# Kernel tuning notes

Measured on AMD Instinct MI355X. Metric: run time of the kernel, lower is better.

## Reference

```python
import jax, jax.numpy as jnp
import numpy as np

D = 512      # d_model
H = 8        # num_heads
HD = D // H  # head_dim = 64
NI = 3       # num_inputs


def setup_inputs() -> dict:
    key = jax.random.key(0)
    ks = jax.random.split(key, 20)
    b, n, ni = 4, 8192, 4096
    s = 0.02
    inp = {
        "x": jax.random.normal(ks[0], (b, n, D), jnp.float32),
        "emb0": jax.random.normal(ks[1], (b, ni, D), jnp.float32),
        "emb1": jax.random.normal(ks[2], (b, ni, D), jnp.float32),
        "emb2": jax.random.normal(ks[3], (b, ni, D), jnp.float32),
        "Wq": jax.random.normal(ks[4], (D, D), jnp.float32) * s,
        "bq": jnp.zeros((D,), jnp.float32),
        "Wk": jax.random.normal(ks[5], (NI, D, D), jnp.float32) * s,
        "bk": jnp.zeros((NI, D), jnp.float32),
        "Wv": jax.random.normal(ks[6], (NI, D, D), jnp.float32) * s,
        "bv": jnp.zeros((NI, D), jnp.float32),
        "Wo": jax.random.normal(ks[7], (D, D), jnp.float32) * s,
        "bo": jnp.zeros((D,), jnp.float32),
        "mask0": jax.random.randint(ks[8], (b, ni), 0, 2).astype(bool),
        "mask1": jax.random.randint(ks[9], (b, ni), 0, 2).astype(bool),
        "mask2": jax.random.randint(ks[10], (b, ni), 0, 2).astype(bool),
    }
    return inp


def _heads(t, b):
    # [b, n, D] -> [b, H, n, HD]
    return t.reshape(b, -1, H, HD).transpose(0, 2, 1, 3)


def reference(x, emb0, emb1, emb2, Wq, bq, Wk, bk, Wv, bv, Wo, bo, mask0, mask1, mask2):
    b, n, _ = x.shape
    q = jax.nn.softmax(_heads(x @ Wq.T + bq, b), axis=-1)  # [b,H,n,HD]
    out = q
    for i, (emb, mask) in enumerate(((emb0, mask0), (emb1, mask1), (emb2, mask2))):
        k = jax.nn.softmax(_heads(emb @ Wk[i].T + bk[i], b), axis=-1)  # [b,H,ni,HD]
        v = _heads(emb @ Wv[i].T + bv[i], b)                            # [b,H,ni,HD]
        k = jnp.where(mask[:, None, :, None], k, 0.0)
        k_sum = k.sum(axis=2, keepdims=True)                            # [b,H,1,HD]
        d_inv = 1.0 / jnp.sum(q * k_sum, axis=-1, keepdims=True)        # [b,H,n,1]
        kv = jnp.einsum('bhsd,bhse->bhde', k, v)                        # [b,H,HD,HD]
        out = out + jnp.einsum('bhnd,bhde->bhne', q, kv) * d_inv
    out = out.transpose(0, 2, 1, 3).reshape(b, n, D) / NI
    return out @ Wo.T + bo
```

## Files before the change

kernel.cpp:

```cpp
#include <hip/hip_runtime.h>

#define D_MODEL 512
#define NH 8
#define HD_ 64
#define NUM_I 3
#define B_ 4
#define NSEQ 8192
#define SSEQ 4096

typedef __attribute__((ext_vector_type(8))) short short8;
typedef __attribute__((ext_vector_type(4))) float floatx4;

static constexpr size_t Q_OFF    = 0;
static constexpr size_t KT_OFF   = 8388608;
static constexpr size_t VT_OFF   = 12582912;
static constexpr size_t XB_OFF   = 8388608;
static constexpr size_t Q2_OFF   = 8388608;
static constexpr size_t EMBB_OFF = 16777216;
static constexpr size_t WB_OFF   = 20971520;
static constexpr size_t KV_OFF   = 22020096;
static constexpr size_t KS_OFF   = 22413312;
static constexpr size_t KVB_OFF  = 22419456;
static constexpr size_t FLAG_OFF = 22616064;

__device__ __forceinline__ float bf2f(unsigned short u) {
    union { unsigned i; float f; } v; v.i = ((unsigned)u) << 16; return v.f;
}
__device__ __forceinline__ unsigned short f2bf(float f) {
    union { float f; unsigned i; } v; v.f = f;
    unsigned r = v.i + 0x7fffu + ((v.i >> 16) & 1u);
    return (unsigned short)(r >> 16);
}
__device__ __forceinline__ void gld16(const void* g, void* l) {
    __builtin_amdgcn_global_load_lds((const __attribute__((address_space(1))) void*)g,
                                     (__attribute__((address_space(3))) void*)l, 16, 0, 0);
}

__global__ void mask_mode_kernel(const int* __restrict__ m, int* __restrict__ flag)
{
    __shared__ int any;
    if (threadIdx.x == 0) any = 0;
    __syncthreads();
    const unsigned v = (unsigned)m[threadIdx.x];
    if (v > 1u) atomicOr(&any, 1);
    __syncthreads();
    if (threadIdx.x == 0) *flag = any;
}

__global__ __launch_bounds__(256)
void f2bf_kernel(const float* __restrict__ in, unsigned short* __restrict__ out, int n8)
{
    const int i = blockIdx.x * 256 + threadIdx.x;
    if (i >= n8) return;
    const float4 a = ((const float4*)in)[2*i];
    const float4 b = ((const float4*)in)[2*i + 1];
    short8 r;
    r[0] = (short)f2bf(a.x); r[1] = (short)f2bf(a.y);
    r[2] = (short)f2bf(a.z); r[3] = (short)f2bf(a.w);
    r[4] = (short)f2bf(b.x); r[5] = (short)f2bf(b.y);
    r[6] = (short)f2bf(b.z); r[7] = (short)f2bf(b.w);
    ((short8*)out)[i] = r;
}

template<int EPI, int OUT>
__global__ __launch_bounds__(256)
void proj_mfma(const unsigned short* __restrict__ A, const unsigned short* __restrict__ W,
               const float* __restrict__ bias, const int* __restrict__ mask,
               const int* __restrict__ maskmode, void* __restrict__ Cv)
{
    __shared__ short smem[(OUT == 2) ? 18432 : 8192];
    short* As = smem;
    short* Bs = smem + 4096;
    const int tid  = threadIdx.x;
    const int wid  = tid >> 6, lane = tid & 63;
    const int wm   = wid & 1,  wn   = wid >> 1;
    const int l15  = lane & 15, lq  = lane >> 4;
    const int m0   = blockIdx.x * 128;
    const int n0   = blockIdx.y * 128;

    floatx4 acc[4][4] = {};

    const int srow = tid & 127;
    const int sks  = tid >> 7;
    const unsigned short* Ag = A + (size_t)(m0 + srow) * D_MODEL + sks * 8;
    const unsigned short* Wg = W + (size_t)(n0 + srow) * D_MODEL + sks * 8;
    short* AsW = As + wid * 512;
    short* BsW = Bs + wid * 512;

    const int aoff = (lq * 128 + wm * 64 + l15) * 8;
    const int boff = (lq * 128 + wn * 64 + l15) * 8;

    for (int k0 = 0; k0 < D_MODEL; k0 += 32) {
        __syncthreads();
        gld16(Ag + k0,      AsW);
        gld16(Ag + k0 + 16, AsW + 2048);
        gld16(Wg + k0,      BsW);
        gld16(Wg + k0 + 16, BsW + 2048);
        __syncthreads();
        short8 af[4], bfv[4];
#pragma unroll
        for (int mt = 0; mt < 4; ++mt) af[mt]  = *(const short8*)&As[aoff + mt * 128];
#pragma unroll
        for (int nt = 0; nt < 4; ++nt) bfv[nt] = *(const short8*)&Bs[boff + nt * 128];
#pragma unroll
        for (int mt = 0; mt < 4; ++mt)
#pragma unroll
            for (int nt = 0; nt < 4; ++nt)
                acc[mt][nt] = __builtin_amdgcn_mfma_f32_16x16x32_bf16(af[mt], bfv[nt], acc[mt][nt], 0, 0, 0);
    }

    float bl[4];
#pragma unroll
    for (int nt = 0; nt < 4; ++nt) bl[nt] = bias[n0 + wn * 64 + nt * 16 + l15];
#pragma unroll
    for (int mt = 0; mt < 4; ++mt)
#pragma unroll
        for (int nt = 0; nt < 4; ++nt)
#pragma unroll
            for (int r = 0; r < 4; ++r) acc[mt][nt][r] += bl[nt];

    if (EPI >= 1) {
#pragma unroll
        for (int mt = 0; mt < 4; ++mt)
#pragma unroll
            for (int r = 0; r < 4; ++r) {
                float mx = fmaxf(fmaxf(acc[mt][0][r], acc[mt][1][r]),
                                 fmaxf(acc[mt][2][r], acc[mt][3][r]));
#pragma unroll
                for (int off = 1; off < 16; off <<= 1) mx = fmaxf(mx, __shfl_xor(mx, off));
                float s = 0.f;
#pragma unroll
                for (int nt = 0; nt < 4; ++nt) {
                    const float e = __expf(acc[mt][nt][r] - mx);
                    acc[mt][nt][r] = e; s += e;
                }
#pragma unroll
                for (int off = 1; off < 16; off <<= 1) s += __shfl_xor(s, off);
                const float inv = 1.f / s;
#pragma unroll
                for (int nt = 0; nt < 4; ++nt) acc[mt][nt][r] *= inv;
            }
    }
    if (EPI == 2) {
        const int bytemode = *maskmode;
#pragma unroll
        for (int mt = 0; mt < 4; ++mt)
#pragma unroll
            for (int r = 0; r < 4; ++r) {
                const int grow = m0 + wm * 64 + mt * 16 + lq * 4 + r;
                const bool keep = bytemode ? (((const unsigned char*)mask)[grow] != 0)
                                           : (mask[grow] != 0);
                if (!keep) {
#pragma unroll
                    for (int nt = 0; nt < 4; ++nt) acc[mt][nt][r] = 0.f;
                }
            }
    }

    if (OUT == 2) {
        __syncthreads();
        short* tw = smem + wid * 4608;
#pragma unroll
        for (int mt = 0; mt < 4; ++mt)
#pragma unroll
            for (int nt = 0; nt < 4; ++nt) {
                ushort4 p;
                p.x = f2bf(acc[mt][nt][0]); p.y = f2bf(acc[mt][nt][1]);
                p.z = f2bf(acc[mt][nt][2]); p.w = f2bf(acc[mt][nt][3]);
                *(ushort4*)&tw[(nt*16 + l15)*72 + mt*16 + lq*4] = p;
            }
        __syncthreads();
        const int b_idx = m0 >> 12;
        const int s_base = (m0 & 4095) + wm * 64;
        const int h = (n0 >> 6) + wn;
        unsigned short* outp = (unsigned short*)Cv +
            ((size_t)(b_idx * NH + h) * 64 + lane) * SSEQ + s_base;
        const short* src = &tw[lane * 72];
#pragma unroll
        for (int sc = 0; sc < 8; ++sc)
            *(short8*)&outp[sc*8] = *(const short8*)&src[sc*8];
    } else {
#pragma unroll
        for (int mt = 0; mt < 4; ++mt)
#pragma unroll
            for (int r = 0; r < 4; ++r) {
                const size_t row = m0 + wm * 64 + mt * 16 + lq * 4 + r;
#pragma unroll
                for (int nt = 0; nt < 4; ++nt) {
                    const int col = n0 + wn * 64 + nt * 16 + l15;
                    if (OUT == 1)
                        ((unsigned short*)Cv)[row * D_MODEL + col] = f2bf(acc[mt][nt][r]);
                    else
                        ((float*)Cv)[row * D_MODEL + col] = acc[mt][nt][r];
                }
            }
    }
}

__global__ __launch_bounds__(256)
void kv_accum_mfma(const unsigned short* __restrict__ kT, const unsigned short* __restrict__ vT,
                   float* __restrict__ kv, float* __restrict__ ksum, int i_idx)
{
    const int chunk = blockIdx.x;
    const int h = blockIdx.y, b = blockIdx.z;
    __shared__ short As[2048];
    __shared__ short Bs[2048];
    const int tid = threadIdx.x;
    const int wid = tid >> 6, lane = tid & 63;
    const int wm  = wid & 1,  wn  = wid >> 1;
    const int l15 = lane & 15, lq = lane >> 4;

    const size_t base = (size_t)(b * NH + h) * 64 * SSEQ + chunk * 512;
    const int srow = tid & 63, ssub = tid >> 6;
    const unsigned short* Ag = vT + base + (size_t)srow * SSEQ + ssub * 8;
    const unsigned short* Bg = kT + base + (size_t)srow * SSEQ + ssub * 8;
    short* AsW = As + wid * 512;
    short* BsW = Bs + wid * 512;

    floatx4 acc[2][2] = {};
    floatx4 ks[2] = {};
    short8 ones;
#pragma unroll
    for (int j = 0; j < 8; ++j) ones[j] = (short)0x3F80;

    const int aoff = (wm*32 + l15)*8;
    const int boff = (wn*32 + l15)*8;

    for (int k0 = 0; k0 < 512; k0 += 32) {
        __syncthreads();
        gld16(Ag + k0, AsW);
        gld16(Bg + k0, BsW);
        __syncthreads();
        short8 af[2], bfr[2];
#pragma unroll
        for (int mt = 0; mt < 2; ++mt) af[mt]  = *(const short8*)&As[lq*512 + aoff + mt*128];
#pragma unroll
        for (int nt = 0; nt < 2; ++nt) bfr[nt] = *(const short8*)&Bs[lq*512 + boff + nt*128];
#pragma unroll
        for (int mt = 0; mt < 2; ++mt)
#pragma unroll
            for (int nt = 0; nt < 2; ++nt)
                acc[mt][nt] = __builtin_amdgcn_mfma_f32_16x16x32_bf16(af[mt], bfr[nt], acc[mt][nt], 0, 0, 0);
        if (wm == 0) {
#pragma unroll
            for (int nt = 0; nt < 2; ++nt)
                ks[nt] = __builtin_amdgcn_mfma_f32_16x16x32_bf16(ones, bfr[nt], ks[nt], 0, 0, 0);
        }
    }
    float* kvb = kv + (size_t)((i_idx*B_ + b)*NH + h) * 4096;
#pragma unroll
    for (int mt = 0; mt < 2; ++mt)
#pragma unroll
        for (int nt = 0; nt < 2; ++nt)
#pragma unroll
            for (int r = 0; r < 4; ++r) {
                const int e = wm*32 + mt*16 + lq*4 + r;
                const int d = wn*32 + nt*16 + l15;
                atomicAdd(&kvb[e*64 + d], acc[mt][nt][r]);
            }
    if (wm == 0 && lq == 0) {
        float* ksb = ksum + (size_t)((i_idx*B_ + b)*NH + h) * 64;
#pragma unroll
        for (int nt = 0; nt < 2; ++nt)
            atomicAdd(&ksb[wn*32 + nt*16 + l15], ks[nt][0]);
    }
}

__global__ __launch_bounds__(256)
void combine_mfma(const unsigned short* __restrict__ Q, const unsigned short* __restrict__ kvT,
                  const float* __restrict__ ksum, unsigned short* __restrict__ Qo)
{
    const int m0 = blockIdx.x * 128;
    const int h  = blockIdx.y;
    const int b  = m0 >> 13;
    __shared__ short qs[8192];
    __shared__ float skl[NUM_I][64];
    __shared__ float dinv[NUM_I][128];
    const int tid = threadIdx.x;
    const int wid = tid >> 6, lane = tid & 63;
    const int l15 = lane & 15, lq = lane >> 4;

    const unsigned short* Qbase = Q + (size_t)m0 * D_MODEL + h * 64;
#pragma unroll
    for (int j = 0; j < 4; ++j) {
        const int g = tid + j * 256;
        const int row = g & 127, c = g >> 7;
        gld16(Qbase + (size_t)row * D_MODEL + c * 8, qs + (size_t)(wid*64 + j*256) * 8);
    }
    if (tid < NUM_I * 64) {
        const int i = tid >> 6, d = tid & 63;
        skl[i][d] = ksum[(size_t)((i*B_ + b)*NH + h) * 64 + d];
    }
    __syncthreads();
    for (int it = tid; it < NUM_I * 128; it += 256) {
        const int i = it >> 7, row = it & 127;
        float s = 0.f;
#pragma unroll
        for (int d = 0; d < 64; ++d)
            s += bf2f((unsigned short)qs[(d >> 3)*1024 + row*8 + (d & 7)]) * skl[i][d];
        dinv[i][row] = 1.f / s;
    }
    __syncthreads();

    short8 af[2][2];
#pragma unroll
    for (int mt = 0; mt < 2; ++mt)
#pragma unroll
        for (int ks = 0; ks < 2; ++ks)
            af[mt][ks] = *(const short8*)&qs[(ks*4 + lq)*1024 + (wid*32 + mt*16 + l15)*8];

    floatx4 accO[2][4] = {};
    for (int i = 0; i < NUM_I; ++i) {
        const unsigned short* kvb = kvT + (size_t)((i*B_ + b)*NH + h) * 4096;
        short8 bfr[4][2];
#pragma unroll
        for (int nt = 0; nt < 4; ++nt)
#pragma unroll
            for (int ks = 0; ks < 2; ++ks)
                bfr[nt][ks] = *(const short8*)&kvb[(nt*16 + l15)*64 + ks*32 + lq*8];
#pragma unroll
        for (int mt = 0; mt < 2; ++mt)
#pragma unroll
            for (int nt = 0; nt < 4; ++nt) {
                floatx4 p = {};
                p = __builtin_amdgcn_mfma_f32_16x16x32_bf16(af[mt][0], bfr[nt][0], p, 0, 0, 0);
                p = __builtin_amdgcn_mfma_f32_16x16x32_bf16(af[mt][1], bfr[nt][1], p, 0, 0, 0);
#pragma unroll
                for (int r = 0; r < 4; ++r) {
                    const int row = wid*32 + mt*16 + lq*4 + r;
                    accO[mt][nt][r] += p[r] * dinv[i][row];
                }
            }
    }
    const float inv3 = 1.f / 3.f;
#pragma unroll
    for (int mt = 0; mt < 2; ++mt)
#pragma unroll
        for (int nt = 0; nt < 4; ++nt)
#pragma unroll
            for (int r = 0; r < 4; ++r) {
                const int row = wid*32 + mt*16 + lq*4 + r;
                const int col = nt*16 + l15;
                const float qv = bf2f((unsigned short)qs[(col >> 3)*1024 + row*8 + (col & 7)]);
                Qo[(size_t)(m0 + row) * D_MODEL + h*64 + col] = f2bf((qv + accO[mt][nt][r]) * inv3);
            }
}

extern "C" void kernel_launch(void* const* d_in, const int* in_sizes, int n_in,
                              void* d_out, int out_size, void* d_ws, size_t ws_size,
                              hipStream_t stream)
{
    const float* x      = (const float*)d_in[0];
    const float* emb[3] = {(const float*)d_in[1], (const float*)d_in[2], (const float*)d_in[3]};
    const float* Wq = (const float*)d_in[4];
    const float* bq = (const float*)d_in[5];
    const float* Wk = (const float*)d_in[6];
    const float* bk = (const float*)d_in[7];
    const float* Wv = (const float*)d_in[8];
    const float* bv = (const float*)d_in[9];
    const float* Wo = (const float*)d_in[10];
    const float* bo = (const float*)d_in[11];
    const int* mask[3] = {(const int*)d_in[12], (const int*)d_in[13], (const int*)d_in[14]};
    float* out = (float*)d_out;

    float* ws = (float*)d_ws;
    unsigned short* qb   = (unsigned short*)(ws + Q_OFF);
    unsigned short* kT   = (unsigned short*)(ws + KT_OFF);
    unsigned short* vT   = (unsigned short*)(ws + VT_OFF);
    unsigned short* xb   = (unsigned short*)(ws + XB_OFF);
    unsigned short* q2b  = (unsigned short*)(ws + Q2_OFF);
    unsigned short* embb = (unsigned short*)(ws + EMBB_OFF);
    unsigned short* wb   = (unsigned short*)(ws + WB_OFF);
    unsigned short* wqb  = wb;
    unsigned short* wkb  = wb + 262144;
    unsigned short* wvb  = wb + 1048576;
    unsigned short* wob  = wb + 1835008;
    float* kv   = ws + KV_OFF;
    float* ksum = ws + KS_OFF;
    unsigned short* kvb16 = (unsigned short*)(ws + KVB_OFF);
    int*   flag = (int*)(ws + FLAG_OFF);

    mask_mode_kernel<<<1, 256, 0, stream>>>(mask[0], flag);
    hipMemsetAsync(kv, 0, (size_t)(NUM_I*B_*NH*HD_*HD_ + NUM_I*B_*NH*HD_) * sizeof(float), stream);

    f2bf_kernel<<<8192, 256, 0, stream>>>(x,  xb,  2097152);
    f2bf_kernel<<<128,  256, 0, stream>>>(Wq, wqb, 32768);
    f2bf_kernel<<<384,  256, 0, stream>>>(Wk, wkb, 98304);
    f2bf_kernel<<<384,  256, 0, stream>>>(Wv, wvb, 98304);
    f2bf_kernel<<<128,  256, 0, stream>>>(Wo, wob, 32768);

    const dim3 gq(B_*NSEQ/128, D_MODEL/128);
    const dim3 gk(B_*SSEQ/128, D_MODEL/128);

    proj_mfma<1, 1><<<gq, 256, 0, stream>>>(xb, wqb, bq, nullptr, nullptr, qb);
    for (int i = 0; i < NUM_I; ++i) {
        f2bf_kernel<<<4096, 256, 0, stream>>>(emb[i], embb, 1048576);
        proj_mfma<2, 2><<<gk, 256, 0, stream>>>(embb, wkb + (size_t)i*262144,
                                                bk + (size_t)i*D_MODEL, mask[i], flag, kT);
        proj_mfma<0, 2><<<gk, 256, 0, stream>>>(embb, wvb + (size_t)i*262144,
                                                bv + (size_t)i*D_MODEL, nullptr, nullptr, vT);
        kv_accum_mfma<<<dim3(8, NH, B_), 256, 0, stream>>>(kT, vT, kv, ksum, i);
    }
    f2bf_kernel<<<192, 256, 0, stream>>>(kv, kvb16, 49152);
    combine_mfma<<<dim3(B_*NSEQ/128, NH), 256, 0, stream>>>(qb, kvb16, ksum, q2b);
    proj_mfma<0, 0><<<gq, 256, 0, stream>>>(q2b, wob, bo, nullptr, nullptr, out);
}
```

Baseline: 581.3 us.

## Fuse fp32-to-bf16 conversion into projection GEMM with LDS-resident weight tile

```diff
diff --git a/kernel.cpp b/kernel.cpp
--- a/kernel.cpp
+++ b/kernel.cpp
@@ -12,16 +12,14 @@
 typedef __attribute__((ext_vector_type(4))) float floatx4;
 
 static constexpr size_t Q_OFF    = 0;
-static constexpr size_t KT_OFF   = 8388608;
-static constexpr size_t VT_OFF   = 12582912;
-static constexpr size_t XB_OFF   = 8388608;
 static constexpr size_t Q2_OFF   = 8388608;
-static constexpr size_t EMBB_OFF = 16777216;
-static constexpr size_t WB_OFF   = 20971520;
-static constexpr size_t KV_OFF   = 22020096;
-static constexpr size_t KS_OFF   = 22413312;
-static constexpr size_t KVB_OFF  = 22419456;
-static constexpr size_t FLAG_OFF = 22616064;
+static constexpr size_t KT_OFF   = 16777216;
+static constexpr size_t VT_OFF   = 20971520;
+static constexpr size_t WB_OFF   = 25165824;
+static constexpr size_t KV_OFF   = 26214400;
+static constexpr size_t KS_OFF   = 26607616;
+static constexpr size_t KVB_OFF  = 26613760;
+static constexpr size_t FLAG_OFF = 26712064;
 
 __device__ __forceinline__ float bf2f(unsigned short u) {
     union { unsigned i; float f; } v; v.i = ((unsigned)u) << 16; return v.f;
@@ -34,6 +32,14 @@
 __device__ __forceinline__ void gld16(const void* g, void* l) {
     __builtin_amdgcn_global_load_lds((const __attribute__((address_space(1))) void*)g,
                                      (__attribute__((address_space(3))) void*)l, 16, 0, 0);
+}
+__device__ __forceinline__ short8 cvt8(const float4& a, const float4& b) {
+    short8 r;
+    r[0] = (short)f2bf(a.x); r[1] = (short)f2bf(a.y);
+    r[2] = (short)f2bf(a.z); r[3] = (short)f2bf(a.w);
+    r[4] = (short)f2bf(b.x); r[5] = (short)f2bf(b.y);
+    r[6] = (short)f2bf(b.z); r[7] = (short)f2bf(b.w);
+    return r;
 }
 
 __global__ void mask_mode_kernel(const int* __restrict__ m, int* __restrict__ flag)
@@ -54,64 +60,111 @@
     if (i >= n8) return;
     const float4 a = ((const float4*)in)[2*i];
     const float4 b = ((const float4*)in)[2*i + 1];
-    short8 r;
-    r[0] = (short)f2bf(a.x); r[1] = (short)f2bf(a.y);
-    r[2] = (short)f2bf(a.z); r[3] = (short)f2bf(a.w);
-    r[4] = (short)f2bf(b.x); r[5] = (short)f2bf(b.y);
-    r[6] = (short)f2bf(b.z); r[7] = (short)f2bf(b.w);
-    ((short8*)out)[i] = r;
-}
-
-template<int EPI, int OUT>
+    ((short8*)out)[i] = cvt8(a, b);
+}
+
+template<int EPI, int OUT, bool AFP32>
 __global__ __launch_bounds__(256)
-void proj_mfma(const unsigned short* __restrict__ A, const unsigned short* __restrict__ W,
-               const float* __restrict__ bias, const int* __restrict__ mask,
-               const int* __restrict__ maskmode, void* __restrict__ Cv)
-{
-    __shared__ short smem[(OUT == 2) ? 18432 : 8192];
-    short* As = smem;
-    short* Bs = smem + 4096;
-    const int tid  = threadIdx.x;
-    const int wid  = tid >> 6, lane = tid & 63;
-    const int wm   = wid & 1,  wn   = wid >> 1;
-    const int l15  = lane & 15, lq  = lane >> 4;
-    const int m0   = blockIdx.x * 128;
-    const int n0   = blockIdx.y * 128;
+void proj2(const void* __restrict__ Av, const unsigned short* __restrict__ W,
+           const float* __restrict__ bias, const int* __restrict__ mask,
+           const int* __restrict__ maskmode, void* __restrict__ Cv)
+{
+    __shared__ short Ws[64 * 520];
+    const int tid = threadIdx.x;
+    const int wid = tid >> 6, lane = tid & 63;
+    const int l15 = lane & 15, lq = lane >> 4;
+    const int m0w = blockIdx.x * 256 + wid * 64;
+    const int n0  = blockIdx.y * 64;
+
+#pragma unroll
+    for (int j = 0; j < 16; ++j) {
+        const int row = wid * 16 + j;
+        gld16(W + (size_t)(n0 + row) * D_MODEL + lane * 8, Ws + row * 520);
+    }
+    __syncthreads();
 
     floatx4 acc[4][4] = {};
-
-    const int srow = tid & 127;
-    const int sks  = tid >> 7;
-    const unsigned short* Ag = A + (size_t)(m0 + srow) * D_MODEL + sks * 8;
-    const unsigned short* Wg = W + (size_t)(n0 + srow) * D_MODEL + sks * 8;
-    short* AsW = As + wid * 512;
-    short* BsW = Bs + wid * 512;
-
-    const int aoff = (lq * 128 + wm * 64 + l15) * 8;
-    const int boff = (lq * 128 + wn * 64 + l15) * 8;
-
-    for (int k0 = 0; k0 < D_MODEL; k0 += 32) {
-        __syncthreads();
-        gld16(Ag + k0,      AsW);
-        gld16(Ag + k0 + 16, AsW + 2048);
-        gld16(Wg + k0,      BsW);
-        gld16(Wg + k0 + 16, BsW + 2048);
-        __syncthreads();
-        short8 af[4], bfv[4];
-#pragma unroll
-        for (int mt = 0; mt < 4; ++mt) af[mt]  = *(const short8*)&As[aoff + mt * 128];
-#pragma unroll
-        for (int nt = 0; nt < 4; ++nt) bfv[nt] = *(const short8*)&Bs[boff + nt * 128];
-#pragma unroll
-        for (int mt = 0; mt < 4; ++mt)
+    const float*          Af = (const float*)Av;
+    const unsigned short* Ab = (const unsigned short*)Av;
+
+    size_t abase[4];
+#pragma unroll
+    for (int mt = 0; mt < 4; ++mt)
+        abase[mt] = (size_t)(m0w + mt * 16 + l15) * D_MODEL + lq * 8;
+
+    short8 afc[4];
+    if (AFP32) {
+        float4 buf[2][4][2];
+#pragma unroll
+        for (int mt = 0; mt < 4; ++mt) {
+            const float4* p0 = (const float4*)(Af + abase[mt]);
+            buf[0][mt][0] = p0[0]; buf[0][mt][1] = p0[1];
+            const float4* p1 = (const float4*)(Af + abase[mt] + 32);
+            buf[1][mt][0] = p1[0]; buf[1][mt][1] = p1[1];
+        }
+#pragma unroll
+        for (int mt = 0; mt < 4; ++mt) afc[mt] = cvt8(buf[0][mt][0], buf[0][mt][1]);
+#pragma unroll
+        for (int kk = 0; kk < 16; ++kk) {
+            const int k0 = kk * 32;
+            if (kk < 14) {
+#pragma unroll
+                for (int mt = 0; mt < 4; ++mt) {
+                    const float4* p = (const float4*)(Af + abase[mt] + k0 + 64);
+                    buf[kk & 1][mt][0] = p[0]; buf[kk & 1][mt][1] = p[1];
+                }
+            }
+            short8 bfr[4];
 #pragma unroll
             for (int nt = 0; nt < 4; ++nt)
-                acc[mt][nt] = __builtin_amdgcn_mfma_f32_16x16x32_bf16(af[mt], bfv[nt], acc[mt][nt], 0, 0, 0);
+                bfr[nt] = *(const short8*)&Ws[(nt * 16 + l15) * 520 + k0 + lq * 8];
+#pragma unroll
+            for (int mt = 0; mt < 4; ++mt)
+#pragma unroll
+                for (int nt = 0; nt < 4; ++nt)
+                    acc[mt][nt] = __builtin_amdgcn_mfma_f32_16x16x32_bf16(afc[mt], bfr[nt], acc[mt][nt], 0, 0, 0);
+            if (kk < 15) {
+#pragma unroll
+                for (int mt = 0; mt < 4; ++mt)
+                    afc[mt] = cvt8(buf[(kk + 1) & 1][mt][0], buf[(kk + 1) & 1][mt][1]);
+            }
+        }
+    } else {
+        short8 buf[2][4];
+#pragma unroll
+        for (int mt = 0; mt < 4; ++mt) {
+            buf[0][mt] = *(const short8*)(Ab + abase[mt]);
+            buf[1][mt] = *(const short8*)(Ab + abase[mt] + 32);
+        }
+#pragma unroll
+        for (int mt = 0; mt < 4; ++mt) afc[mt] = buf[0][mt];
+#pragma unroll
+        for (int kk = 0; kk < 16; ++kk) {
+            const int k0 = kk * 32;
+            if (kk < 14) {
+#pragma unroll
+                for (int mt = 0; mt < 4; ++mt)
+                    buf[kk & 1][mt] = *(const short8*)(Ab + abase[mt] + k0 + 64);
+            }
+            short8 bfr[4];
+#pragma unroll
+            for (int nt = 0; nt < 4; ++nt)
+                bfr[nt] = *(const short8*)&Ws[(nt * 16 + l15) * 520 + k0 + lq * 8];
+#pragma unroll
+            for (int mt = 0; mt < 4; ++mt)
+#pragma unroll
+                for (int nt = 0; nt < 4; ++nt)
+                    acc[mt][nt] = __builtin_amdgcn_mfma_f32_16x16x32_bf16(afc[mt], bfr[nt], acc[mt][nt], 0, 0, 0);
+            if (kk < 15) {
+#pragma unroll
+                for (int mt = 0; mt < 4; ++mt) afc[mt] = buf[(kk + 1) & 1][mt];
+            }
+        }
     }
 
     float bl[4];
 #pragma unroll
-    for (int nt = 0; nt < 4; ++nt) bl[nt] = bias[n0 + wn * 64 + nt * 16 + l15];
+    for (int nt = 0; nt < 4; ++nt) bl[nt] = bias[n0 + nt * 16 + l15];
 #pragma unroll
     for (int mt = 0; mt < 4; ++mt)
 #pragma unroll
@@ -147,7 +200,7 @@
         for (int mt = 0; mt < 4; ++mt)
 #pragma unroll
             for (int r = 0; r < 4; ++r) {
-                const int grow = m0 + wm * 64 + mt * 16 + lq * 4 + r;
+                const int grow = m0w + mt * 16 + lq * 4 + r;
                 const bool keep = bytemode ? (((const unsigned char*)mask)[grow] != 0)
                                            : (mask[grow] != 0);
                 if (!keep) {
@@ -159,7 +212,7 @@
 
     if (OUT == 2) {
         __syncthreads();
-        short* tw = smem + wid * 4608;
+        short* tw = Ws + wid * 4608;
 #pragma unroll
         for (int mt = 0; mt < 4; ++mt)
 #pragma unroll
@@ -167,27 +220,27 @@
                 ushort4 p;
                 p.x = f2bf(acc[mt][nt][0]); p.y = f2bf(acc[mt][nt][1]);
                 p.z = f2bf(acc[mt][nt][2]); p.w = f2bf(acc[mt][nt][3]);
-                *(ushort4*)&tw[(nt*16 + l15)*72 + mt*16 + lq*4] = p;
+                *(ushort4*)&tw[(nt * 16 + l15) * 72 + mt * 16 + lq * 4] = p;
             }
         __syncthreads();
-        const int b_idx = m0 >> 12;
-        const int s_base = (m0 & 4095) + wm * 64;
-        const int h = (n0 >> 6) + wn;
+        const int b_idx  = m0w >> 12;
+        const int s_base = m0w & 4095;
+        const int h = blockIdx.y;
         unsigned short* outp = (unsigned short*)Cv +
             ((size_t)(b_idx * NH + h) * 64 + lane) * SSEQ + s_base;
         const short* src = &tw[lane * 72];
 #pragma unroll
         for (int sc = 0; sc < 8; ++sc)
-            *(short8*)&outp[sc*8] = *(const short8*)&src[sc*8];
+            *(short8*)&outp[sc * 8] = *(const short8*)&src[sc * 8];
     } else {
 #pragma unroll
         for (int mt = 0; mt < 4; ++mt)
 #pragma unroll
             for (int r = 0; r < 4; ++r) {
-                const size_t row = m0 + wm * 64 + mt * 16 + lq * 4 + r;
+                const size_t row = m0w + mt * 16 + lq * 4 + r;
 #pragma unroll
                 for (int nt = 0; nt < 4; ++nt) {
-                    const int col = n0 + wn * 64 + nt * 16 + l15;
+                    const int col = n0 + nt * 16 + l15;
                     if (OUT == 1)
                         ((unsigned short*)Cv)[row * D_MODEL + col] = f2bf(acc[mt][nt][r]);
                     else
@@ -365,11 +418,9 @@
 
     float* ws = (float*)d_ws;
     unsigned short* qb   = (unsigned short*)(ws + Q_OFF);
+    unsigned short* q2b  = (unsigned short*)(ws + Q2_OFF);
     unsigned short* kT   = (unsigned short*)(ws + KT_OFF);
     unsigned short* vT   = (unsigned short*)(ws + VT_OFF);
-    unsigned short* xb   = (unsigned short*)(ws + XB_OFF);
-    unsigned short* q2b  = (unsigned short*)(ws + Q2_OFF);
-    unsigned short* embb = (unsigned short*)(ws + EMBB_OFF);
     unsigned short* wb   = (unsigned short*)(ws + WB_OFF);
     unsigned short* wqb  = wb;
     unsigned short* wkb  = wb + 262144;
@@ -383,25 +434,23 @@
     mask_mode_kernel<<<1, 256, 0, stream>>>(mask[0], flag);
     hipMemsetAsync(kv, 0, (size_t)(NUM_I*B_*NH*HD_*HD_ + NUM_I*B_*NH*HD_) * sizeof(float), stream);
 
-    f2bf_kernel<<<8192, 256, 0, stream>>>(x,  xb,  2097152);
-    f2bf_kernel<<<128,  256, 0, stream>>>(Wq, wqb, 32768);
-    f2bf_kernel<<<384,  256, 0, stream>>>(Wk, wkb, 98304);
-    f2bf_kernel<<<384,  256, 0, stream>>>(Wv, wvb, 98304);
-    f2bf_kernel<<<128,  256, 0, stream>>>(Wo, wob, 32768);
-
-    const dim3 gq(B_*NSEQ/128, D_MODEL/128);
-    const dim3 gk(B_*SSEQ/128, D_MODEL/128);
-
-    proj_mfma<1, 1><<<gq, 256, 0, stream>>>(xb, wqb, bq, nullptr, nullptr, qb);
+    f2bf_kernel<<<128, 256, 0, stream>>>(Wq, wqb, 32768);
+    f2bf_kernel<<<384, 256, 0, stream>>>(Wk, wkb, 98304);
+    f2bf_kernel<<<384, 256, 0, stream>>>(Wv, wvb, 98304);
+    f2bf_kernel<<<128, 256, 0, stream>>>(Wo, wob, 32768);
+
+    const dim3 gq(B_*NSEQ/256, NH);
+    const dim3 gk(B_*SSEQ/256, NH);
+
+    proj2<1, 1, true ><<<gq, 256, 0, stream>>>(x, wqb, bq, nullptr, nullptr, qb);
     for (int i = 0; i < NUM_I; ++i) {
-        f2bf_kernel<<<4096, 256, 0, stream>>>(emb[i], embb, 1048576);
-        proj_mfma<2, 2><<<gk, 256, 0, stream>>>(embb, wkb + (size_t)i*262144,
-                                                bk + (size_t)i*D_MODEL, mask[i], flag, kT);
-        proj_mfma<0, 2><<<gk, 256, 0, stream>>>(embb, wvb + (size_t)i*262144,
-                                                bv + (size_t)i*D_MODEL, nullptr, nullptr, vT);
+        proj2<2, 2, true ><<<gk, 256, 0, stream>>>(emb[i], wkb + (size_t)i*262144,
+                                                   bk + (size_t)i*D_MODEL, mask[i], flag, kT);
+        proj2<0, 2, true ><<<gk, 256, 0, stream>>>(emb[i], wvb + (size_t)i*262144,
+                                                   bv + (size_t)i*D_MODEL, nullptr, nullptr, vT);
         kv_accum_mfma<<<dim3(8, NH, B_), 256, 0, stream>>>(kT, vT, kv, ksum, i);
     }
     f2bf_kernel<<<192, 256, 0, stream>>>(kv, kvb16, 49152);
     combine_mfma<<<dim3(B_*NSEQ/128, NH), 256, 0, stream>>>(qb, kvb16, ksum, q2b);
-    proj_mfma<0, 0><<<gq, 256, 0, stream>>>(q2b, wob, bo, nullptr, nullptr, out);
-}
+    proj2<0, 0, false><<<gq, 256, 0, stream>>>(q2b, wob, bo, nullptr, nullptr, out);
+}
```

Result: slower. 679.7 us (+16.9%).
